# Kernel optimization log

Measured on AMD Instinct MI355X. Metric: run time of the kernel, lower is better.

## Reference

```python
import jax, jax.numpy as jnp
import numpy as np

NUM_FEATURE = 128  # bins; linear in_features = NUM_FEATURE + 1
VECTOR_DIM = 64


def setup_inputs() -> dict:
    key = jax.random.key(0)
    k1, k2, k3 = jax.random.split(key, 3)
    x = jax.random.randint(k1, (8192, 200), 0, NUM_FEATURE + 1)
    # nn.Linear(num_feature+1, vector_dim): W is (out, in) = (64, 129)
    W = jax.random.normal(k2, (VECTOR_DIM, NUM_FEATURE + 1), dtype=jnp.float32) * 0.05
    b = jax.random.normal(k3, (VECTOR_DIM,), dtype=jnp.float32) * 0.05
    return {"x": x, "W": W, "b": b}


def reference(x, W, b):
    # embeddings = tril(ones)[x] has ones in columns 0..x (inclusive), so
    # embeddings @ W.T = sum_{j<=x} W[:, j] = cumsum(W, axis=1)[:, x].
    # This avoids materializing the (..., F+1) one-hot-prefix tensor.
    Wc = jnp.cumsum(W, axis=1)              # (D, F+1)
    out = jnp.take(Wc.T, x, axis=0) + b     # (8192, 200, D)
    return out
```

## Files before the change

### kernel.cpp

```cpp
#include <hip/hip_runtime.h>


constexpr int F1   = 129;
constexpr int D    = 64;
constexpr int ROWS = 8192 * 200;
constexpr int TBL_F = F1 * D;
constexpr int TBL4  = TBL_F / 4;

constexpr int BLOCKS = 1024;
constexpr int TPB    = 512;
constexpr int ROWS_PER_BLOCK = ROWS / BLOCKS;
constexpr int Q_PER_BLOCK    = ROWS_PER_BLOCK * D / 4;
constexpr int ITERS          = Q_PER_BLOCK / TPB;

typedef float floatx4 __attribute__((ext_vector_type(4)));

__global__ __launch_bounds__(256) void build_table_kernel(
        const float* __restrict__ W,
        const float* __restrict__ b,
        float* __restrict__ tbl) {
    __shared__ float ldsW[TBL_F];
    for (int i = threadIdx.x; i < TBL_F; i += 256)
        ldsW[i] = W[i];
    __syncthreads();
    int d = threadIdx.x;
    if (d < D) {
        float acc = b[d];
        for (int j = 0; j < F1; ++j) {
            acc += ldsW[d * F1 + j];
            tbl[j * D + d] = acc;
        }
    }
}

__global__ __launch_bounds__(TPB, 8) void embed_main_kernel(
        const int* __restrict__ x,
        const float* __restrict__ tbl,
        float* __restrict__ out) {
    __shared__ floatx4 lds_tbl[TBL4];
    __shared__ int     lds_x[ROWS_PER_BLOCK];

    const floatx4* t4 = (const floatx4*)tbl;
    for (int i = threadIdx.x; i < TBL4; i += TPB)
        lds_tbl[i] = t4[i];
    const int row0 = blockIdx.x * ROWS_PER_BLOCK;
    for (int i = threadIdx.x; i < ROWS_PER_BLOCK; i += TPB)
        lds_x[i] = x[row0 + i];
    __syncthreads();

    floatx4* out4 = (floatx4*)out + (size_t)blockIdx.x * Q_PER_BLOCK;
#pragma unroll 5
    for (int it = 0; it < ITERS; ++it) {
        int j    = it * TPB + threadIdx.x;
        int xi   = lds_x[j >> 4];
        floatx4 v = lds_tbl[xi * 16 + (j & 15)];
        out4[j] = v;
    }
}

extern "C" void kernel_launch(void* const* d_in, const int* in_sizes, int n_in,
                              void* d_out, int out_size, void* d_ws, size_t ws_size,
                              hipStream_t stream) {
    const int*   x = (const int*)  d_in[0];
    const float* W = (const float*)d_in[1];
    const float* b = (const float*)d_in[2];
    float* out = (float*)d_out;
    float* tbl = (float*)d_ws;

    build_table_kernel<<<1, 256, 0, stream>>>(W, b, tbl);
    embed_main_kernel<<<BLOCKS, TPB, 0, stream>>>(x, tbl, out);
}
```

Baseline: 420.8 us.

## Fuse cumsum table build into main embedding kernel, computing table per block in LDS

Removes the separate single-block table-build kernel and its launch plus workspace round-trip. Each block now has 64 threads compute the prefix-sum table straight into LDS from W and b, while the other threads load x. This drops one launch and the serialized single-block pre-pass, at the cost of redundant per-block compute: a 129-step serial chain over strided global reads of W that the rest of the block waits on.

```diff
diff --git a/kernel.cpp b/kernel.cpp
--- a/kernel.cpp
+++ b/kernel.cpp
@@ -15,37 +15,36 @@
 
 typedef float floatx4 __attribute__((ext_vector_type(4)));
 
-__global__ __launch_bounds__(256) void build_table_kernel(
+__global__ __launch_bounds__(TPB, 8) void embed_fused_kernel(
+        const int*   __restrict__ x,
         const float* __restrict__ W,
         const float* __restrict__ b,
-        float* __restrict__ tbl) {
-    __shared__ float ldsW[TBL_F];
-    for (int i = threadIdx.x; i < TBL_F; i += 256)
-        ldsW[i] = W[i];
-    __syncthreads();
-    int d = threadIdx.x;
-    if (d < D) {
-        float acc = b[d];
-        for (int j = 0; j < F1; ++j) {
-            acc += ldsW[d * F1 + j];
-            tbl[j * D + d] = acc;
-        }
-    }
-}
-
-__global__ __launch_bounds__(TPB, 8) void embed_main_kernel(
-        const int* __restrict__ x,
-        const float* __restrict__ tbl,
-        float* __restrict__ out) {
+        float*       __restrict__ out) {
     __shared__ floatx4 lds_tbl[TBL4];
     __shared__ int     lds_x[ROWS_PER_BLOCK];
+    float* tblf = (float*)lds_tbl;
 
-    const floatx4* t4 = (const floatx4*)tbl;
-    for (int i = threadIdx.x; i < TBL4; i += TPB)
-        lds_tbl[i] = t4[i];
     const int row0 = blockIdx.x * ROWS_PER_BLOCK;
     for (int i = threadIdx.x; i < ROWS_PER_BLOCK; i += TPB)
         lds_x[i] = x[row0 + i];
+
+    if (threadIdx.x < D) {
+        const int d = threadIdx.x;
+        const float* wrow = W + d * F1;
+        float acc = b[d];
+        int j = 0;
+#pragma unroll 1
+        for (int c = 0; c < 16; ++c) {
+            float v[8];
+#pragma unroll
+            for (int i = 0; i < 8; ++i) v[i] = wrow[j + i];
+#pragma unroll
+            for (int i = 0; i < 8; ++i) { acc += v[i]; tblf[(j + i) * D + d] = acc; }
+            j += 8;
+        }
+        acc += wrow[128];
+        tblf[128 * D + d] = acc;
+    }
     __syncthreads();
 
     floatx4* out4 = (floatx4*)out + (size_t)blockIdx.x * Q_PER_BLOCK;
@@ -65,8 +64,7 @@
     const float* W = (const float*)d_in[1];
     const float* b = (const float*)d_in[2];
     float* out = (float*)d_out;
-    float* tbl = (float*)d_ws;
+    (void)d_ws; (void)ws_size;
 
-    build_table_kernel<<<1, 256, 0, stream>>>(W, b, tbl);
-    embed_main_kernel<<<BLOCKS, TPB, 0, stream>>>(x, tbl, out);
+    embed_fused_kernel<<<BLOCKS, TPB, 0, stream>>>(x, W, b, out);
 }
```

Result: no change. 420.3 us (-0.1%).
